# Kernel optimization log

Hardware: AMD Instinct MI355X
Metric: run time of the kernel (lower is better)

## Reference

```python
import itertools
import jax, jax.numpy as jnp
import numpy as np

LATENT_DIM = 8
N = 2 * LATENT_DIM  # width of z_combined = concat([z, dz])
BATCH = 131072

# Static combinatorial index sets, matching the nested-loop order
# (i <= j [<= k]) of the torch implementation exactly.
_PAIRS = np.array(list(itertools.combinations_with_replacement(range(N), 2)), dtype=np.int32)   # [136, 2]
_TRIPLES = np.array(list(itertools.combinations_with_replacement(range(N), 3)), dtype=np.int32)  # [816, 3]


def setup_inputs() -> dict:
    key = jax.random.key(0)
    k1, k2 = jax.random.split(key)
    z = jax.random.normal(k1, (BATCH, LATENT_DIM), dtype=jnp.float32)
    dz = jax.random.normal(k2, (BATCH, LATENT_DIM), dtype=jnp.float32)
    return {"z": z, "dz": dz}


def reference(z, dz):
    # z, dz: [B, latent_dim] -> Theta: [B, 985]
    zc = jnp.concatenate([z, dz], axis=1)  # [B, N]
    B = zc.shape[0]
    ones = jnp.ones((B, 1), dtype=zc.dtype)
    # degree-2 terms: zc[:, i] * zc[:, j] for i <= j, all at once via gather
    deg2 = zc[:, _PAIRS[:, 0]] * zc[:, _PAIRS[:, 1]]  # [B, 136]
    # degree-3 terms: zc[:, i] * zc[:, j] * zc[:, k] for i <= j <= k
    deg3 = zc[:, _TRIPLES[:, 0]] * zc[:, _TRIPLES[:, 1]] * zc[:, _TRIPLES[:, 2]]  # [B, 816]
    sine = jnp.sin(zc)  # [B, N]
    return jnp.concatenate([ones, zc, deg2, deg3, sine], axis=1)  # [B, 985]
```

## Files before the change

kernel.cpp:

```cpp
#include <hip/hip_runtime.h>
#include <cstddef>

#define NDIM   16
#define NTAB   969
#define NCOLS  985
#define RPW    16
#define SLOT   17

__global__ __launch_bounds__(256) void sindy_kernel(const float* __restrict__ z,
                                                    const float* __restrict__ dz,
                                                    float* __restrict__ out, int batch) {
  __shared__ unsigned short tab[NTAB];
  __shared__ float zs[4][SLOT];

  for (int e = threadIdx.x; e < NTAB; e += 256) {
    int i = 16, j = 16, k = 16;
    if (e >= 1 && e <= 16) {
      i = e - 1;
    } else if (e >= 17 && e < 153) {
      int p = e - 17; i = 0;
      while (p >= 16 - i) { p -= 16 - i; ++i; }
      j = i + p;
    } else if (e >= 153) {
      int t = e - 153; i = 0;
      for (;;) { int c = (16 - i) * (17 - i) / 2; if (t < c) break; t -= c; ++i; }
      j = i;
      while (t >= 16 - j) { t -= 16 - j; ++j; }
      k = j + t;
    }
    tab[e] = (unsigned short)(i | (j << 5) | (k << 10));
  }
  __syncthreads();

  const int w = threadIdx.x >> 6;
  const int l = threadIdx.x & 63;
  float* zr = zs[w];

  const int rbase = (blockIdx.x * 4 + w) * RPW;

  for (int rr = 0; rr < RPW; ++rr) {
    const int row = rbase + rr;
    if (row >= batch) break;

    if (l < SLOT) {
      float v = 1.0f;
      if (l < 8)       v = z[(size_t)row * 8 + l];
      else if (l < 16) v = dz[(size_t)row * 8 + (l - 8)];
      zr[l] = v;
    }

    float* orow = out + (size_t)row * NCOLS;

    #pragma unroll
    for (int it = 0; it < 15; ++it) {
      const int col = it * 64 + l;
      const unsigned pk = tab[col];
      const float v = zr[pk & 31] * zr[(pk >> 5) & 31] * zr[(pk >> 10) & 31];
      orow[col] = v;
    }

    if (l < NCOLS - 960) {
      const int col = 960 + l;
      float v;
      if (col < NTAB) {
        const unsigned pk = tab[col];
        v = zr[pk & 31] * zr[(pk >> 5) & 31] * zr[(pk >> 10) & 31];
      } else {
        v = __sinf(zr[col - NTAB]);
      }
      orow[col] = v;
    }
  }
}

extern "C" void kernel_launch(void* const* d_in, const int* in_sizes, int n_in,
                              void* d_out, int out_size, void* d_ws, size_t ws_size,
                              hipStream_t stream) {
  const float* z  = (const float*)d_in[0];
  const float* dz = (const float*)d_in[1];
  float* out = (float*)d_out;
  const int batch = in_sizes[0] / 8;

  const int blocks = (batch + 4 * RPW - 1) / (4 * RPW);
  sindy_kernel<<<blocks, 256, 0, stream>>>(z, dz, out, batch);
}
```

Measured before the change: 127.0 us.

## Build degree-2 products in LDS and form each output from one product

The kernel now writes the 136 pairwise products of each row, plus the ones, z and sine values, into a per-wave LDS row. Every output column then becomes a single product of two LDS entries (degree-3 terms reuse the precomputed pair), replacing the three-way gather. The per-lane index words are loaded once into registers instead of being read from LDS on every row. The goal is fewer LDS reads and multiplies per column, at the cost of an extra LDS build phase per row with scheduling barriers and no explicit wave-level sync between the build and the read.

```diff
diff --git a/kernel.cpp b/kernel.cpp
--- a/kernel.cpp
+++ b/kernel.cpp
@@ -1,75 +1,89 @@
 #include <hip/hip_runtime.h>
 #include <cstddef>
 
-#define NDIM   16
-#define NTAB   969
-#define NCOLS  985
-#define RPW    16
-#define SLOT   17
+#define NCOLS 985
+#define RPW   16
+#define GSTR  176
 
 __global__ __launch_bounds__(256) void sindy_kernel(const float* __restrict__ z,
                                                     const float* __restrict__ dz,
                                                     float* __restrict__ out, int batch) {
-  __shared__ unsigned short tab[NTAB];
-  __shared__ float zs[4][SLOT];
+  __shared__ unsigned short mtab[1024];
+  __shared__ unsigned short ptab[136];
+  __shared__ float G[4][GSTR];
 
-  for (int e = threadIdx.x; e < NTAB; e += 256) {
-    int i = 16, j = 16, k = 16;
-    if (e >= 1 && e <= 16) {
-      i = e - 1;
-    } else if (e >= 17 && e < 153) {
-      int p = e - 17; i = 0;
-      while (p >= 16 - i) { p -= 16 - i; ++i; }
-      j = i + p;
-    } else if (e >= 153) {
-      int t = e - 153; i = 0;
+  const int tid = threadIdx.x;
+
+  for (int e = tid; e < 1024; e += 256) {
+    int a, b;
+    if (e < 153)       { a = (e == 0) ? 0 : e; b = 0; }
+    else if (e < 969)  {
+      int t = e - 153, i = 0;
       for (;;) { int c = (16 - i) * (17 - i) / 2; if (t < c) break; t -= c; ++i; }
-      j = i;
-      while (t >= 16 - j) { t -= 16 - j; ++j; }
-      k = j + t;
+      int j = i; while (t >= 16 - j) { t -= 16 - j; ++j; }
+      int k = j + t;
+      int p = i * 16 - i * (i - 1) / 2 + (j - i);
+      a = 17 + p; b = 1 + k;
     }
-    tab[e] = (unsigned short)(i | (j << 5) | (k << 10));
+    else if (e < 985)  { a = 153 + (e - 969); b = 0; }
+    else               { a = 169; b = 169; }
+    mtab[e] = (unsigned short)(a | (b << 8));
+  }
+  for (int e = tid; e < 136; e += 256) {
+    int p = e, i = 0; while (p >= 16 - i) { p -= 16 - i; ++i; }
+    ptab[e] = (unsigned short)(i | ((i + p) << 4));
   }
   __syncthreads();
 
-  const int w = threadIdx.x >> 6;
-  const int l = threadIdx.x & 63;
-  float* zr = zs[w];
+  const int w = tid >> 6, l = tid & 63;
 
-  const int rbase = (blockIdx.x * 4 + w) * RPW;
+  unsigned short mt[16];
+  #pragma unroll
+  for (int wd = 0; wd < 16; ++wd) mt[wd] = mtab[wd * 64 + l];
+  const unsigned pe0 = ptab[l];
+  const unsigned pe1 = ptab[64 + l];
+  const unsigned pe2 = ptab[(128 + l < 136) ? (128 + l) : 135];
+
+  float* Gw = G[w];
+  const int row0 = (blockIdx.x * 4 + w) * RPW;
+  if (row0 >= batch) return;
 
   for (int rr = 0; rr < RPW; ++rr) {
-    const int row = rbase + rr;
+    const int row = row0 + rr;
     if (row >= batch) break;
 
-    if (l < SLOT) {
-      float v = 1.0f;
-      if (l < 8)       v = z[(size_t)row * 8 + l];
-      else if (l < 16) v = dz[(size_t)row * 8 + (l - 8)];
-      zr[l] = v;
+    float gval = 0.f;
+    if (l == 0)       gval = 1.0f;
+    else if (l < 9)   gval = z [(size_t)row * 8 + (l - 1)];
+    else if (l < 17)  gval = dz[(size_t)row * 8 + (l - 9)];
+    const int gaddr = (l < 17) ? l : (152 + l);
+    if (l < 24) Gw[gaddr] = gval;
+
+    const float sv = __shfl(gval, l + 1);
+    if (l < 16) Gw[153 + l] = __sinf(sv);
+    __builtin_amdgcn_sched_barrier(0);
+
+    {
+      float a0 = Gw[1 + (pe0 & 15)], b0 = Gw[1 + (pe0 >> 4)];
+      Gw[17 + l] = a0 * b0;
+      float a1 = Gw[1 + (pe1 & 15)], b1 = Gw[1 + (pe1 >> 4)];
+      Gw[17 + 64 + l] = a1 * b1;
+      if (l < 8) {
+        float a2 = Gw[1 + (pe2 & 15)], b2 = Gw[1 + (pe2 >> 4)];
+        Gw[17 + 128 + l] = a2 * b2;
+      }
     }
+    __builtin_amdgcn_sched_barrier(0);
 
     float* orow = out + (size_t)row * NCOLS;
-
     #pragma unroll
-    for (int it = 0; it < 15; ++it) {
-      const int col = it * 64 + l;
-      const unsigned pk = tab[col];
-      const float v = zr[pk & 31] * zr[(pk >> 5) & 31] * zr[(pk >> 10) & 31];
-      orow[col] = v;
+    for (int wd = 0; wd < 16; ++wd) {
+      const unsigned e = mt[wd];
+      const float v = Gw[e & 255] * Gw[e >> 8];
+      if (wd < 15)                 orow[wd * 64 + l] = v;
+      else if (l < NCOLS - 960)    orow[960 + l] = v;
     }
-
-    if (l < NCOLS - 960) {
-      const int col = 960 + l;
-      float v;
-      if (col < NTAB) {
-        const unsigned pk = tab[col];
-        v = zr[pk & 31] * zr[(pk >> 5) & 31] * zr[(pk >> 10) & 31];
-      } else {
-        v = __sinf(zr[col - NTAB]);
-      }
-      orow[col] = v;
-    }
+    __builtin_amdgcn_sched_barrier(0);
   }
 }
 
```

New measurement: 128.9 us. Within noise of the previous version (+1.5%).

## Use flat float4 output stream with shared degree-2 table and double-buffered staging

Applied to the files above, without the earlier changes.

Replaces the per-row, per-lane scalar store loop with a persistent grid that treats the output as a flat float4 stream. Each float4 is built by multiplying two entries from a precomputed per-row table of degree-≤2 terms held in shared memory. That table is staged with a double buffer so loading the next rows overlaps with the current stores. The goal is fully coalesced 16-byte stores and fewer shared reads per element. The cost is magic-number division, a barrier on every iteration, and reliance on batch being divisible by 4.

```diff
diff --git a/kernel.cpp b/kernel.cpp
--- a/kernel.cpp
+++ b/kernel.cpp
@@ -1,75 +1,149 @@
 #include <hip/hip_runtime.h>
 #include <cstddef>
 
-#define NDIM   16
-#define NTAB   969
-#define NCOLS  985
-#define RPW    16
-#define SLOT   17
+#define TPB   256
+#define NBLK  1024
+#define GSTR  176
+#define GSLOT (3 * GSTR)
+
+__device__ __forceinline__ unsigned divn(unsigned f) {
+  return (unsigned)(((unsigned long long)f * 4465021839ULL) >> 42);
+}
+
+__device__ __forceinline__ float ldzc(const float* __restrict__ z,
+                                      const float* __restrict__ dz,
+                                      int row, int i) {
+  const float* p = (i < 8) ? (z + (size_t)row * 8 + i)
+                           : (dz + (size_t)row * 8 + (i - 8));
+  return *p;
+}
+
+__device__ __forceinline__ float gval(int type, float a, float b) {
+  if (type == 2) return a * b;
+  if (type == 1) return a;
+  if (type == 3) return __sinf(a);
+  if (type == 0) return 1.0f;
+  return 0.0f;
+}
 
 __global__ __launch_bounds__(256) void sindy_kernel(const float* __restrict__ z,
                                                     const float* __restrict__ dz,
-                                                    float* __restrict__ out, int batch) {
-  __shared__ unsigned short tab[NTAB];
-  __shared__ float zs[4][SLOT];
+                                                    float* __restrict__ out,
+                                                    int batch, int niters,
+                                                    unsigned totalU) {
+  __shared__ alignas(8) ushort4 qtab[985];
+  __shared__ unsigned short ktab[GSTR];
+  __shared__ float G[2][GSLOT];
 
-  for (int e = threadIdx.x; e < NTAB; e += 256) {
-    int i = 16, j = 16, k = 16;
-    if (e >= 1 && e <= 16) {
-      i = e - 1;
-    } else if (e >= 17 && e < 153) {
-      int p = e - 17; i = 0;
-      while (p >= 16 - i) { p -= 16 - i; ++i; }
-      j = i + p;
-    } else if (e >= 153) {
-      int t = e - 153; i = 0;
-      for (;;) { int c = (16 - i) * (17 - i) / 2; if (t < c) break; t -= c; ++i; }
-      j = i;
-      while (t >= 16 - j) { t -= 16 - j; ++j; }
-      k = j + t;
+  const int tid = threadIdx.x;
+  const int bid = blockIdx.x;
+
+  for (int e = tid; e < GSTR; e += TPB) {
+    int i = 0, j = 0, type;
+    if (e == 0)        type = 0;
+    else if (e < 17)  { type = 1; i = e - 1; }
+    else if (e < 153) { type = 2; int p = e - 17; while (p >= 16 - i) { p -= 16 - i; ++i; } j = i + p; }
+    else if (e < 169) { type = 3; i = e - 153; }
+    else               type = 4;
+    ktab[e] = (unsigned short)(i | (j << 4) | (type << 8));
+  }
+
+  for (int q = tid; q < 985; q += TPB) {
+    int c0 = 4 * q;
+    while (c0 >= 985) c0 -= 985;
+    unsigned short ent[4];
+    #pragma unroll
+    for (int k = 0; k < 4; ++k) {
+      const int inc = (c0 + k >= 985) ? 1 : 0;
+      const int c   = c0 + k - inc * 985;
+      unsigned goff, midx;
+      if (c < 153)      { goff = (unsigned)c; midx = 0; }
+      else if (c < 969) {
+        int t = c - 153, i = 0;
+        for (;;) { int cn = (16 - i) * (17 - i) / 2; if (t < cn) break; t -= cn; ++i; }
+        goff = (unsigned)(17 + (136 - (16 - i) * (17 - i) / 2) + t);
+        midx = (unsigned)(1 + i);
+      } else { goff = (unsigned)(153 + (c - 969)); midx = 0; }
+      ent[k] = (unsigned short)(goff | (midx << 8) | (inc << 13));
     }
-    tab[e] = (unsigned short)(i | (j << 5) | (k << 10));
+    qtab[q] = make_ushort4(ent[0], ent[1], ent[2], ent[3]);
   }
   __syncthreads();
 
-  const int w = threadIdx.x >> 6;
-  const int l = threadIdx.x & 63;
-  float* zr = zs[w];
+  const int lr0 = tid / GSTR,  id0 = tid - lr0 * GSTR;
+  const int e1i = tid + 256;
+  const int lr1 = e1i / GSTR,  id1 = e1i - lr1 * GSTR;
+  const bool has2 = (tid + 512 < GSLOT);
+  const unsigned kt0 = ktab[id0];
+  const unsigned kt1 = ktab[id1];
+  const unsigned kt2 = has2 ? ktab[tid + 512 - 2 * GSTR] : 0x0400u;
+  const int i0 = kt0 & 15, j0 = (kt0 >> 4) & 15, ty0 = kt0 >> 8;
+  const int i1 = kt1 & 15, j1 = (kt1 >> 4) & 15, ty1 = kt1 >> 8;
+  const int i2 = kt2 & 15, j2 = (kt2 >> 4) & 15, ty2 = kt2 >> 8;
 
-  const int rbase = (blockIdx.x * 4 + w) * RPW;
+  {
+    const unsigned F0 = (unsigned)bid * 1024u;
+    const int rmin = (int)divn(F0);
+    const int r0 = min(rmin + lr0, batch - 1);
+    const int r1 = min(rmin + lr1, batch - 1);
+    const int r2 = min(rmin + 2,   batch - 1);
+    const float a0 = ldzc(z, dz, r0, i0), b0 = ldzc(z, dz, r0, j0);
+    const float a1 = ldzc(z, dz, r1, i1), b1 = ldzc(z, dz, r1, j1);
+    float a2 = 0.f, b2 = 0.f;
+    if (has2) { a2 = ldzc(z, dz, r2, i2); b2 = ldzc(z, dz, r2, j2); }
+    G[0][tid]       = gval(ty0, a0, b0);
+    G[0][tid + 256] = gval(ty1, a1, b1);
+    if (has2) G[0][tid + 512] = gval(ty2, a2, b2);
+  }
+  __syncthreads();
 
-  for (int rr = 0; rr < RPW; ++rr) {
-    const int row = rbase + rr;
-    if (row >= batch) break;
+  for (int it = 0; it < niters; ++it) {
+    const int cur = it & 1, nxt = cur ^ 1;
 
-    if (l < SLOT) {
-      float v = 1.0f;
-      if (l < 8)       v = z[(size_t)row * 8 + l];
-      else if (l < 16) v = dz[(size_t)row * 8 + (l - 8)];
-      zr[l] = v;
+    const bool dostage = (it + 1 < niters);
+    float a0, b0, a1, b1, a2 = 0.f, b2 = 0.f;
+    if (dostage) {
+      const unsigned F0n = (unsigned)(it + 1) * 1048576u + (unsigned)bid * 1024u;
+      const int rminN = (int)divn(F0n);
+      const int r0 = min(rminN + lr0, batch - 1);
+      const int r1 = min(rminN + lr1, batch - 1);
+      const int r2 = min(rminN + 2,   batch - 1);
+      a0 = ldzc(z, dz, r0, i0); b0 = ldzc(z, dz, r0, j0);
+      a1 = ldzc(z, dz, r1, i1); b1 = ldzc(z, dz, r1, j1);
+      if (has2) { a2 = ldzc(z, dz, r2, i2); b2 = ldzc(z, dz, r2, j2); }
     }
 
-    float* orow = out + (size_t)row * NCOLS;
-
-    #pragma unroll
-    for (int it = 0; it < 15; ++it) {
-      const int col = it * 64 + l;
-      const unsigned pk = tab[col];
-      const float v = zr[pk & 31] * zr[(pk >> 5) & 31] * zr[(pk >> 10) & 31];
-      orow[col] = v;
+    const unsigned U = (unsigned)it * (NBLK * TPB) + (unsigned)bid * TPB + (unsigned)tid;
+    if (U < totalU) {
+      const unsigned f0   = U * 4u;
+      const unsigned row0 = divn(f0);
+      const unsigned q    = U - divn(U) * 985u;
+      const unsigned rmin = divn((unsigned)it * 1048576u + (unsigned)bid * 1024u);
+      const unsigned r0b  = (row0 - rmin) * GSTR;
+      const ushort4 e = qtab[q];
+      const float* Gc = G[cur];
+      float4 v;
+      { const unsigned g = e.x, bb = r0b + ((g & 0x2000u) ? GSTR : 0u);
+        v.x = Gc[bb + (g & 0xffu)] * Gc[bb + ((g >> 8) & 0x1fu)]; }
+      { const unsigned g = e.y, bb = r0b + ((g & 0x2000u) ? GSTR : 0u);
+        v.y = Gc[bb + (g & 0xffu)] * Gc[bb + ((g >> 8) & 0x1fu)]; }
+      { const unsigned g = e.z, bb = r0b + ((g & 0x2000u) ? GSTR : 0u);
+        v.z = Gc[bb + (g & 0xffu)] * Gc[bb + ((g >> 8) & 0x1fu)]; }
+      { const unsigned g = e.w, bb = r0b + ((g & 0x2000u) ? GSTR : 0u);
+        v.w = Gc[bb + (g & 0xffu)] * Gc[bb + ((g >> 8) & 0x1fu)]; }
+      *(float4*)(out + (size_t)f0) = v;
     }
 
-    if (l < NCOLS - 960) {
-      const int col = 960 + l;
-      float v;
-      if (col < NTAB) {
-        const unsigned pk = tab[col];
-        v = zr[pk & 31] * zr[(pk >> 5) & 31] * zr[(pk >> 10) & 31];
-      } else {
-        v = __sinf(zr[col - NTAB]);
-      }
-      orow[col] = v;
+    if (dostage) {
+      G[nxt][tid]       = gval(ty0, a0, b0);
+      G[nxt][tid + 256] = gval(ty1, a1, b1);
+      if (has2) G[nxt][tid + 512] = gval(ty2, a2, b2);
     }
+
+    asm volatile("s_waitcnt lgkmcnt(0)" ::: "memory");
+    __builtin_amdgcn_sched_barrier(0);
+    __builtin_amdgcn_s_barrier();
+    __builtin_amdgcn_sched_barrier(0);
   }
 }
 
@@ -81,6 +155,7 @@
   float* out = (float*)d_out;
   const int batch = in_sizes[0] / 8;
 
-  const int blocks = (batch + 4 * RPW - 1) / (4 * RPW);
-  sindy_kernel<<<blocks, 256, 0, stream>>>(z, dz, out, batch);
+  const unsigned totalU = (unsigned)(batch / 4) * 985u;
+  const int niters = (int)((totalU + (unsigned)(NBLK * TPB) - 1) / (unsigned)(NBLK * TPB));
+  sindy_kernel<<<NBLK, TPB, 0, stream>>>(z, dz, out, batch, niters, totalU);
 }
```

Measured after the change: 219.0 us. +72.4%, slower.
